# Kernel tuning notes

Measured on AMD Instinct MI355X. Metric: run time of the kernel, lower is better.

The kernel has to match this reference:

```python
import jax, jax.numpy as jnp
import numpy as np

B, S, D = 8, 2048, 512
FF = 2048
E = 8

def setup_inputs() -> dict:
    key = jax.random.key(0)
    ks = jax.random.split(key, 7)
    s = 1.0 / np.sqrt(D)
    sf = 1.0 / np.sqrt(FF)
    return {
        "x":  jax.random.normal(ks[0], (B, S, D), dtype=jnp.float32),
        "Wg": jax.random.uniform(ks[1], (D, E), jnp.float32, -s, s),
        "bg": jax.random.uniform(ks[2], (E,), jnp.float32, -s, s),
        "W1": jax.random.uniform(ks[3], (E, D, FF), jnp.float32, -s, s),
        "b1": jax.random.uniform(ks[4], (E, FF), jnp.float32, -s, s),
        "W2": jax.random.uniform(ks[5], (E, FF, D), jnp.float32, -sf, sf),
        "b2": jax.random.uniform(ks[6], (E, D), jnp.float32, -sf, sf),
    }

def reference(x, Wg, bg, W1, b1, W2, b2):
    b, s, d = x.shape
    xf = x.reshape(-1, d)                      # [T, D]
    logits = xf @ Wg + bg                      # [T, E]
    probs = jax.nn.softmax(logits, axis=-1)
    pmax = jnp.max(probs, axis=-1)             # [T]
    routes = jnp.argmax(probs, axis=-1)        # [T] int
    xs = xf * pmax[:, None]                    # scale tokens by router prob
    # per-expert FFN over all tokens, select the routed expert's output
    out_tok = jnp.zeros_like(xf)
    for e in range(E):
        h = jax.nn.relu(xs @ W1[e] + b1[e])    # [T, FF]
        y = h @ W2[e] + b2[e]                  # [T, D]
        out_tok = jnp.where((routes == e)[:, None], y, out_tok)
    # torch.cat of per-expert nonzero-index gathers == tokens stably sorted by expert id
    order = jnp.argsort(routes)                # jnp.argsort is stable
    return out_tok[order].reshape(b, s, d)
```

## Files before the change

### kernel.cpp

```cpp
#include <hip/hip_runtime.h>
#include <hip/hip_bf16.h>

constexpr int TTOK  = 16384;
constexpr int DDIM  = 512;
constexpr int FFDIM = 2048;
constexpr int NEXP  = 8;
constexpr int GB_TOK = 16;
constexpr int NGB    = TTOK / GB_TOK;
constexpr int MAXTILES = TTOK / 128 + NEXP;
constexpr int PREP_GATE = NGB;
constexpr int PREP_TR   = 16 * 1024;

typedef __attribute__((ext_vector_type(8))) short short8_t;
typedef __attribute__((ext_vector_type(4))) float f32x4_t;

__device__ __forceinline__ unsigned short f2bf(float f) {
    union { float f; unsigned u; } v; v.f = f;
    return (unsigned short)((v.u + 0x7fffu + ((v.u >> 16) & 1u)) >> 16);
}

__device__ __forceinline__ void gl_lds16(const void* g, void* l) {
    __builtin_amdgcn_global_load_lds(
        (const __attribute__((address_space(1))) void*)g,
        (__attribute__((address_space(3))) void*)l,
        16, 0, 0);
}

__global__ __launch_bounds__(256) void prep_kernel(const float* __restrict__ x,
                                                   const float* __restrict__ Wg,
                                                   const float* __restrict__ bg,
                                                   int* __restrict__ route,
                                                   float* __restrict__ pmax,
                                                   int* __restrict__ blockCounts,
                                                   const float* __restrict__ W1,
                                                   const float* __restrict__ W2,
                                                   unsigned short* __restrict__ W1T,
                                                   unsigned short* __restrict__ W2T) {
    int tid = threadIdx.x;
    if (blockIdx.x >= PREP_GATE) {
        __shared__ float tile[32][33];
        int id = blockIdx.x - PREP_GATE;
        int z = id >> 10;
        int t = id & 1023;
        bool isW2 = z >= NEXP;
        int e = isW2 ? z - NEXP : z;
        int R = isW2 ? FFDIM : DDIM;
        int C = isW2 ? DDIM : FFDIM;
        int tilesC = C / 32;
        int c0 = (t % tilesC) * 32;
        int r0 = (t / tilesC) * 32;
        const float* s = (isW2 ? W2 : W1) + (size_t)e * DDIM * FFDIM;
        unsigned short* d = (isW2 ? W2T : W1T) + (size_t)e * DDIM * FFDIM;
        int tx = tid & 31, ty = tid >> 5;
        #pragma unroll
        for (int i = 0; i < 4; i++)
            tile[ty + 8 * i][tx] = s[(size_t)(r0 + ty + 8 * i) * C + c0 + tx];
        __syncthreads();
        #pragma unroll
        for (int i = 0; i < 4; i++)
            d[(size_t)(c0 + ty + 8 * i) * R + r0 + tx] = f2bf(tile[tx][ty + 8 * i]);
        return;
    }
    __shared__ int cnt[NEXP];
    __shared__ float bgs[NEXP];
    int gb = blockIdx.x;
    if (tid < NEXP) { cnt[tid] = 0; bgs[tid] = bg[tid]; }
    __syncthreads();
    int wave = tid >> 6, lane = tid & 63;
    float w[8][8];
    #pragma unroll
    for (int jj = 0; jj < 8; jj++) {
        float4 a = *(const float4*)(Wg + (size_t)(lane * 8 + jj) * NEXP);
        float4 b = *(const float4*)(Wg + (size_t)(lane * 8 + jj) * NEXP + 4);
        w[jj][0] = a.x; w[jj][1] = a.y; w[jj][2] = a.z; w[jj][3] = a.w;
        w[jj][4] = b.x; w[jj][5] = b.y; w[jj][6] = b.z; w[jj][7] = b.w;
    }
    int tbase = gb * GB_TOK + wave * 4;
    for (int it = 0; it < 4; it++) {
        int t = tbase + it;
        float4 xa = *(const float4*)(x + (size_t)t * DDIM + lane * 8);
        float4 xb = *(const float4*)(x + (size_t)t * DDIM + lane * 8 + 4);
        float xs[8] = {xa.x, xa.y, xa.z, xa.w, xb.x, xb.y, xb.z, xb.w};
        double acc[NEXP];
        #pragma unroll
        for (int e = 0; e < NEXP; e++) acc[e] = 0.0;
        #pragma unroll
        for (int jj = 0; jj < 8; jj++) {
            double xv = (double)xs[jj];
            #pragma unroll
            for (int e = 0; e < NEXP; e++) acc[e] += xv * (double)w[jj][e];
        }
        #pragma unroll
        for (int off = 32; off > 0; off >>= 1) {
            #pragma unroll
            for (int e = 0; e < NEXP; e++) acc[e] += __shfl_down(acc[e], off);
        }
        if (lane == 0) {
            double l[NEXP];
            #pragma unroll
            for (int e = 0; e < NEXP; e++) l[e] = acc[e] + (double)bgs[e];
            int r = 0; double lm = l[0];
            #pragma unroll
            for (int e = 1; e < NEXP; e++) if (l[e] > lm) { lm = l[e]; r = e; }
            double s = 0.0;
            #pragma unroll
            for (int e = 0; e < NEXP; e++) s += exp(l[e] - lm);
            route[t] = r;
            pmax[t] = (float)(1.0 / s);
            atomicAdd(&cnt[r], 1);
        }
    }
    __syncthreads();
    if (tid < NEXP) blockCounts[gb * NEXP + tid] = cnt[tid];
}

__global__ __launch_bounds__(1024) void scan_kernel(const int* __restrict__ blockCounts,
                                                    int* __restrict__ blockOffsets,
                                                    int* __restrict__ segPrefix,
                                                    int* __restrict__ tilePrefix) {
    int b = threadIdx.x, lane = b & 63, wv = b >> 6;
    int c[NEXP], s[NEXP];
    #pragma unroll
    for (int e = 0; e < NEXP; e++) { c[e] = blockCounts[b * NEXP + e]; s[e] = c[e]; }
    #pragma unroll
    for (int off = 1; off < 64; off <<= 1) {
        #pragma unroll
        for (int e = 0; e < NEXP; e++) {
            int t = __shfl_up(s[e], off);
            if (lane >= off) s[e] += t;
        }
    }
    __shared__ int wtot[16][NEXP];
    __shared__ int wpre[16][NEXP];
    __shared__ int base[NEXP + 1];
    if (lane == 63) {
        #pragma unroll
        for (int e = 0; e < NEXP; e++) wtot[wv][e] = s[e];
    }
    __syncthreads();
    if (wv == 0) {
        int t[NEXP];
        #pragma unroll
        for (int e = 0; e < NEXP; e++) t[e] = (lane < 16) ? wtot[lane][e] : 0;
        #pragma unroll
        for (int off = 1; off < 16; off <<= 1) {
            #pragma unroll
            for (int e = 0; e < NEXP; e++) {
                int u = __shfl_up(t[e], off);
                if (lane >= off) t[e] += u;
            }
        }
        if (lane < 16) {
            #pragma unroll
            for (int e = 0; e < NEXP; e++) wpre[lane][e] = t[e] - wtot[lane][e];
        }
        if (lane == 15) {
            int ssum = 0;
            #pragma unroll
            for (int e = 0; e < NEXP; e++) { base[e] = ssum; segPrefix[e] = ssum; ssum += t[e]; }
            base[NEXP] = ssum; segPrefix[NEXP] = ssum;
            int tp = 0; tilePrefix[0] = 0;
            #pragma unroll
            for (int e = 0; e < NEXP; e++) { tp += (t[e] + 127) >> 7; tilePrefix[e + 1] = tp; }
        }
    }
    __syncthreads();
    #pragma unroll
    for (int e = 0; e < NEXP; e++)
        blockOffsets[b * NEXP + e] = base[e] + wpre[wv][e] + s[e] - c[e];
}

__global__ __launch_bounds__(256) void scatter_kernel(const float* __restrict__ x,
                                                      const int* __restrict__ route,
                                                      const float* __restrict__ pmax,
                                                      const int* __restrict__ blockOffsets,
                                                      unsigned short* __restrict__ Xs) {
    __shared__ int dstL[GB_TOK];
    __shared__ float pmL[GB_TOK];
    int tid = threadIdx.x;
    int bb = blockIdx.x;
    if (tid < GB_TOK) {
        int t = bb * GB_TOK + tid;
        int r = route[t];
        unsigned long long ltmask = (tid == 0) ? 0ull : ((~0ull) >> (64 - tid));
        int rank = 0;
        #pragma unroll
        for (int e = 0; e < NEXP; e++) {
            unsigned long long m = __ballot(r == e);
            if (r == e) rank = __popcll(m & ltmask);
        }
        dstL[tid] = blockOffsets[bb * NEXP + r] + rank;
        pmL[tid] = pmax[t];
    }
    __syncthreads();
    int wave = tid >> 6, lane = tid & 63;
    for (int rr = 0; rr < 4; rr++) {
        int rowl = wave * 4 + rr;
        int t = bb * GB_TOK + rowl;
        float pm = pmL[rowl];
        const float4* xr = (const float4*)(x + (size_t)t * DDIM) + lane * 2;
        float4 a = xr[0], b = xr[1];
        union { short8_t v; unsigned short s[8]; } o;
        o.s[0] = f2bf(a.x * pm); o.s[1] = f2bf(a.y * pm);
        o.s[2] = f2bf(a.z * pm); o.s[3] = f2bf(a.w * pm);
        o.s[4] = f2bf(b.x * pm); o.s[5] = f2bf(b.y * pm);
        o.s[6] = f2bf(b.z * pm); o.s[7] = f2bf(b.w * pm);
        *(short8_t*)(Xs + (size_t)dstL[rowl] * DDIM + lane * 8) = o.v;
    }
}

template <bool RELU, typename OutT, int K, int N>
__global__ __launch_bounds__(256) void gemm_seg(const unsigned short* __restrict__ A,
                                                const unsigned short* __restrict__ Bt,
                                                const float* __restrict__ bias,
                                                OutT* __restrict__ C,
                                                const int* __restrict__ segPrefix,
                                                const int* __restrict__ tilePrefix) {
    int bx = blockIdx.x;
    bx = (bx & 7) * (MAXTILES / 8) + (bx >> 3);
    int t = bx;
    if (t >= tilePrefix[NEXP]) return;
    int e = 0;
    #pragma unroll
    for (int i = 1; i <= NEXP; i++) e += (t >= tilePrefix[i]) ? 1 : 0;
    int seg1 = segPrefix[e + 1];
    int m0 = segPrefix[e] + (t - tilePrefix[e]) * 128;
    int n0 = blockIdx.y * 128;

    __shared__ unsigned short As[2 * 4096];
    __shared__ unsigned short Bs[2 * 4096];

    int tid = threadIdx.x, wave = tid >> 6, lane = tid & 63;
    const unsigned short* Bte = Bt + (size_t)e * N * K;

    int srow = lane >> 2;
    int sg   = (lane & 3) ^ ((lane >> 2) & 3) ^ ((lane >> 4) & 3);
    int scol = sg * 8;

    f32x4_t acc[4][4];
    #pragma unroll
    for (int i = 0; i < 4; i++)
        #pragma unroll
        for (int j = 0; j < 4; j++) acc[i][j] = (f32x4_t){0.f, 0.f, 0.f, 0.f};

    int wm = (wave & 1) * 64;
    int wn = (wave >> 1) * 64;
    int frow = lane & 15;
    int gr = lane >> 4;
    int fswz = (gr ^ (frow & 3) ^ ((frow >> 2) & 3)) * 8;

    int reg0 = wave * 2;
    int arow0 = m0 + reg0 * 16 + srow;
    arow0 = arow0 < TTOK ? arow0 : TTOK - 1;
    int arow1 = m0 + (reg0 + 1) * 16 + srow;
    arow1 = arow1 < TTOK ? arow1 : TTOK - 1;
    const unsigned short* aptr0 = A + (size_t)arow0 * K + scol;
    const unsigned short* aptr1 = A + (size_t)arow1 * K + scol;
    const unsigned short* bptr0 = Bte + (size_t)(n0 + reg0 * 16 + srow) * K + scol;
    const unsigned short* bptr1 = Bte + (size_t)(n0 + (reg0 + 1) * 16 + srow) * K + scol;

    #pragma unroll
    for (int kc = 0; kc < K; kc += 64) {
        #pragma unroll
        for (int p = 0; p < 2; p++) {
            gl_lds16(aptr0 + kc + p * 32, &As[p * 4096 + reg0 * 512]);
            gl_lds16(aptr1 + kc + p * 32, &As[p * 4096 + (reg0 + 1) * 512]);
            gl_lds16(bptr0 + kc + p * 32, &Bs[p * 4096 + reg0 * 512]);
            gl_lds16(bptr1 + kc + p * 32, &Bs[p * 4096 + (reg0 + 1) * 512]);
        }
        __syncthreads();
        #pragma unroll
        for (int p = 0; p < 2; p++) {
            short8_t af[4], bfr[4];
            #pragma unroll
            for (int i = 0; i < 4; i++)
                af[i] = *(const short8_t*)&As[p * 4096 + (wm + i * 16 + frow) * 32 + fswz];
            #pragma unroll
            for (int j = 0; j < 4; j++)
                bfr[j] = *(const short8_t*)&Bs[p * 4096 + (wn + j * 16 + frow) * 32 + fswz];
            #pragma unroll
            for (int i = 0; i < 4; i++)
                #pragma unroll
                for (int j = 0; j < 4; j++)
                    acc[i][j] = __builtin_amdgcn_mfma_f32_16x16x32_bf16(af[i], bfr[j], acc[i][j], 0, 0, 0);
        }
        __syncthreads();
    }

    int quad = lane >> 4;
    int colb = lane & 15;
    float bv[4];
    #pragma unroll
    for (int j = 0; j < 4; j++) bv[j] = bias[(size_t)e * N + n0 + wn + j * 16 + colb];

    if constexpr (sizeof(OutT) == 2) {
        unsigned short* cbuf = As;
        #pragma unroll
        for (int p = 0; p < 2; p++) {
            __syncthreads();
            if ((wave >> 1) == p) {
                #pragma unroll
                for (int i = 0; i < 4; i++)
                    #pragma unroll
                    for (int j = 0; j < 4; j++)
                        #pragma unroll
                        for (int r = 0; r < 4; r++) {
                            float v = acc[i][j][r] + bv[j];
                            if (RELU) v = fmaxf(v, 0.0f);
                            int wrow = wm + i * 16 + quad * 4 + r;
                            int cc = (j * 16 + colb) ^ (((wrow >> 3) & 1) * 16);
                            cbuf[wrow * 72 + cc] = f2bf(v);
                        }
            }
            __syncthreads();
            int row = tid >> 1, ch = (tid & 1) * 32;
            int grow = m0 + row;
            if (grow < seg1) {
                #pragma unroll
                for (int k = 0; k < 4; k++) {
                    int vv = (ch + k * 8) ^ (((row >> 3) & 1) * 16);
                    short8_t v = *(const short8_t*)&cbuf[row * 72 + vv];
                    *(short8_t*)&C[(size_t)grow * N + n0 + p * 64 + ch + k * 8] = v;
                }
            }
        }
    } else {
        #pragma unroll
        for (int i = 0; i < 4; i++) {
            #pragma unroll
            for (int j = 0; j < 4; j++) {
                int col = n0 + wn + j * 16 + colb;
                #pragma unroll
                for (int r = 0; r < 4; r++) {
                    int row = m0 + wm + i * 16 + quad * 4 + r;
                    if (row < seg1) {
                        float v = acc[i][j][r] + bv[j];
                        if (RELU) v = fmaxf(v, 0.0f);
                        C[(size_t)row * N + col] = v;
                    }
                }
            }
        }
    }
}

extern "C" void kernel_launch(void* const* d_in, const int* in_sizes, int n_in,
                              void* d_out, int out_size, void* d_ws, size_t ws_size,
                              hipStream_t stream) {
    const float* x  = (const float*)d_in[0];
    const float* Wg = (const float*)d_in[1];
    const float* bg = (const float*)d_in[2];
    const float* W1 = (const float*)d_in[3];
    const float* b1 = (const float*)d_in[4];
    const float* W2 = (const float*)d_in[5];
    const float* b2 = (const float*)d_in[6];
    float* out = (float*)d_out;

    char* ws = (char*)d_ws;
    size_t off = 0;
    auto alloc = [&](size_t bytes) -> char* {
        char* p = ws + off;
        off += (bytes + 255) & ~(size_t)255;
        return p;
    };
    unsigned short* W1T = (unsigned short*)alloc((size_t)NEXP * DDIM * FFDIM * 2);
    unsigned short* W2T = (unsigned short*)alloc((size_t)NEXP * DDIM * FFDIM * 2);
    unsigned short* Xs  = (unsigned short*)alloc((size_t)TTOK * DDIM * 2);
    unsigned short* H   = (unsigned short*)alloc((size_t)TTOK * FFDIM * 2);
    int*   route        = (int*)alloc((size_t)TTOK * 4);
    float* pmaxArr      = (float*)alloc((size_t)TTOK * 4);
    int*   blockCounts  = (int*)alloc((size_t)NGB * NEXP * 4);
    int*   blockOffsets = (int*)alloc((size_t)NGB * NEXP * 4);
    int*   segPrefix    = (int*)alloc((size_t)(NEXP + 1) * 4);
    int*   tilePrefix   = (int*)alloc((size_t)(NEXP + 1) * 4);

    prep_kernel<<<PREP_GATE + PREP_TR, 256, 0, stream>>>(
        x, Wg, bg, route, pmaxArr, blockCounts, W1, W2, W1T, W2T);
    scan_kernel<<<1, NGB, 0, stream>>>(blockCounts, blockOffsets, segPrefix, tilePrefix);
    scatter_kernel<<<NGB, 256, 0, stream>>>(x, route, pmaxArr, blockOffsets, Xs);
    gemm_seg<true, unsigned short, DDIM, FFDIM><<<dim3(MAXTILES, FFDIM / 128, 1), 256, 0, stream>>>(
        Xs, W1T, b1, H, segPrefix, tilePrefix);
    gemm_seg<false, float, FFDIM, DDIM><<<dim3(MAXTILES, DDIM / 128, 1), 256, 0, stream>>>(
        H, W2T, b2, out, segPrefix, tilePrefix);
}
```

Measured before the change: 311.2 us.

## Move W2 transpose into GEMM1 launch and widen transpose tiles

```diff
diff --git a/kernel.cpp b/kernel.cpp
--- a/kernel.cpp
+++ b/kernel.cpp
@@ -8,8 +8,8 @@
 constexpr int GB_TOK = 16;
 constexpr int NGB    = TTOK / GB_TOK;
 constexpr int MAXTILES = TTOK / 128 + NEXP;
-constexpr int PREP_GATE = NGB;
-constexpr int PREP_TR   = 16 * 1024;
+constexpr int TRW1_BLOCKS = 4096;
+constexpr int TRW2_XBLK   = 256;
 
 typedef __attribute__((ext_vector_type(8))) short short8_t;
 typedef __attribute__((ext_vector_type(4))) float f32x4_t;
@@ -24,6 +24,35 @@
         (const __attribute__((address_space(1))) void*)g,
         (__attribute__((address_space(3))) void*)l,
         16, 0, 0);
+}
+
+__device__ __forceinline__ void tr_tile(const float* __restrict__ src,
+                                        unsigned short* __restrict__ dst,
+                                        int R, int C, int tileId, float* lds) {
+    int tilesC = C / 32;
+    int c0 = (tileId % tilesC) * 32;
+    int r0 = (tileId / tilesC) * 64;
+    int t = threadIdx.x;
+    int lr = t >> 3;
+    int ls = t & 7;
+    #pragma unroll
+    for (int rb = 0; rb < 2; rb++) {
+        int row = rb * 32 + lr;
+        float4 v = *(const float4*)(src + (size_t)(r0 + row) * C + c0 + 4 * ls);
+        int p4 = (4 * ls) ^ (8 * ((row >> 3) & 3));
+        *(float4*)(lds + row * 36 + p4) = v;
+    }
+    __syncthreads();
+    int c = t >> 3;
+    int b = t & 7;
+    union { short8_t v; unsigned short s[8]; } o;
+    #pragma unroll
+    for (int j = 0; j < 8; j++) {
+        int r = 8 * b + j;
+        int p = c ^ (8 * ((r >> 3) & 3));
+        o.s[j] = f2bf(lds[r * 36 + p]);
+    }
+    *(short8_t*)(dst + (size_t)(c0 + c) * R + r0 + 8 * b) = o.v;
 }
 
 __global__ __launch_bounds__(256) void prep_kernel(const float* __restrict__ x,
@@ -33,32 +62,15 @@
                                                    float* __restrict__ pmax,
                                                    int* __restrict__ blockCounts,
                                                    const float* __restrict__ W1,
-                                                   const float* __restrict__ W2,
-                                                   unsigned short* __restrict__ W1T,
-                                                   unsigned short* __restrict__ W2T) {
+                                                   unsigned short* __restrict__ W1T) {
     int tid = threadIdx.x;
-    if (blockIdx.x >= PREP_GATE) {
-        __shared__ float tile[32][33];
-        int id = blockIdx.x - PREP_GATE;
-        int z = id >> 10;
-        int t = id & 1023;
-        bool isW2 = z >= NEXP;
-        int e = isW2 ? z - NEXP : z;
-        int R = isW2 ? FFDIM : DDIM;
-        int C = isW2 ? DDIM : FFDIM;
-        int tilesC = C / 32;
-        int c0 = (t % tilesC) * 32;
-        int r0 = (t / tilesC) * 32;
-        const float* s = (isW2 ? W2 : W1) + (size_t)e * DDIM * FFDIM;
-        unsigned short* d = (isW2 ? W2T : W1T) + (size_t)e * DDIM * FFDIM;
-        int tx = tid & 31, ty = tid >> 5;
-        #pragma unroll
-        for (int i = 0; i < 4; i++)
-            tile[ty + 8 * i][tx] = s[(size_t)(r0 + ty + 8 * i) * C + c0 + tx];
-        __syncthreads();
-        #pragma unroll
-        for (int i = 0; i < 4; i++)
-            d[(size_t)(c0 + ty + 8 * i) * R + r0 + tx] = f2bf(tile[tx][ty + 8 * i]);
+    if (blockIdx.x >= NGB) {
+        __shared__ __align__(16) float tlds[64 * 36];
+        int id = blockIdx.x - NGB;
+        int e = id >> 9;
+        int tile = id & 511;
+        tr_tile(W1 + (size_t)e * DDIM * FFDIM, W1T + (size_t)e * DDIM * FFDIM,
+                DDIM, FFDIM, tile, tlds);
         return;
     }
     __shared__ int cnt[NEXP];
@@ -209,6 +221,135 @@
     }
 }
 
+__global__ __launch_bounds__(256) void gemm1_fused(const unsigned short* __restrict__ A,
+                                                   const unsigned short* __restrict__ Bt,
+                                                   const float* __restrict__ bias,
+                                                   unsigned short* __restrict__ C,
+                                                   const int* __restrict__ segPrefix,
+                                                   const int* __restrict__ tilePrefix,
+                                                   const float* __restrict__ W2,
+                                                   unsigned short* __restrict__ W2T) {
+    constexpr int K = DDIM, N = FFDIM;
+    __shared__ __align__(16) unsigned short SMEM[16384];
+
+    if (blockIdx.x >= MAXTILES) {
+        int id = (blockIdx.x - MAXTILES) * 16 + blockIdx.y;
+        int e = id >> 9;
+        int tile = id & 511;
+        tr_tile(W2 + (size_t)e * DDIM * FFDIM, W2T + (size_t)e * DDIM * FFDIM,
+                FFDIM, DDIM, tile, (float*)SMEM);
+        return;
+    }
+
+    int bx = blockIdx.x;
+    bx = (bx & 7) * (MAXTILES / 8) + (bx >> 3);
+    int t = bx;
+    if (t >= tilePrefix[NEXP]) return;
+    int e = 0;
+    #pragma unroll
+    for (int i = 1; i <= NEXP; i++) e += (t >= tilePrefix[i]) ? 1 : 0;
+    int seg1 = segPrefix[e + 1];
+    int m0 = segPrefix[e] + (t - tilePrefix[e]) * 128;
+    int n0 = blockIdx.y * 128;
+
+    unsigned short* As = SMEM;
+    unsigned short* Bs = SMEM + 8192;
+
+    int tid = threadIdx.x, wave = tid >> 6, lane = tid & 63;
+    const unsigned short* Bte = Bt + (size_t)e * N * K;
+
+    int srow = lane >> 2;
+    int sg   = (lane & 3) ^ ((lane >> 2) & 3) ^ ((lane >> 4) & 3);
+    int scol = sg * 8;
+
+    f32x4_t acc[4][4];
+    #pragma unroll
+    for (int i = 0; i < 4; i++)
+        #pragma unroll
+        for (int j = 0; j < 4; j++) acc[i][j] = (f32x4_t){0.f, 0.f, 0.f, 0.f};
+
+    int wm = (wave & 1) * 64;
+    int wn = (wave >> 1) * 64;
+    int frow = lane & 15;
+    int gr = lane >> 4;
+    int fswz = (gr ^ (frow & 3) ^ ((frow >> 2) & 3)) * 8;
+
+    int reg0 = wave * 2;
+    int arow0 = m0 + reg0 * 16 + srow;
+    arow0 = arow0 < TTOK ? arow0 : TTOK - 1;
+    int arow1 = m0 + (reg0 + 1) * 16 + srow;
+    arow1 = arow1 < TTOK ? arow1 : TTOK - 1;
+    const unsigned short* aptr0 = A + (size_t)arow0 * K + scol;
+    const unsigned short* aptr1 = A + (size_t)arow1 * K + scol;
+    const unsigned short* bptr0 = Bte + (size_t)(n0 + reg0 * 16 + srow) * K + scol;
+    const unsigned short* bptr1 = Bte + (size_t)(n0 + (reg0 + 1) * 16 + srow) * K + scol;
+
+    #pragma unroll
+    for (int kc = 0; kc < K; kc += 64) {
+        #pragma unroll
+        for (int p = 0; p < 2; p++) {
+            gl_lds16(aptr0 + kc + p * 32, &As[p * 4096 + reg0 * 512]);
+            gl_lds16(aptr1 + kc + p * 32, &As[p * 4096 + (reg0 + 1) * 512]);
+            gl_lds16(bptr0 + kc + p * 32, &Bs[p * 4096 + reg0 * 512]);
+            gl_lds16(bptr1 + kc + p * 32, &Bs[p * 4096 + (reg0 + 1) * 512]);
+        }
+        __syncthreads();
+        #pragma unroll
+        for (int p = 0; p < 2; p++) {
+            short8_t af[4], bfr[4];
+            #pragma unroll
+            for (int i = 0; i < 4; i++)
+                af[i] = *(const short8_t*)&As[p * 4096 + (wm + i * 16 + frow) * 32 + fswz];
+            #pragma unroll
+            for (int j = 0; j < 4; j++)
+                bfr[j] = *(const short8_t*)&Bs[p * 4096 + (wn + j * 16 + frow) * 32 + fswz];
+            #pragma unroll
+            for (int i = 0; i < 4; i++)
+                #pragma unroll
+                for (int j = 0; j < 4; j++)
+                    acc[i][j] = __builtin_amdgcn_mfma_f32_16x16x32_bf16(af[i], bfr[j], acc[i][j], 0, 0, 0);
+        }
+        __syncthreads();
+    }
+
+    int quad = lane >> 4;
+    int colb = lane & 15;
+    float bv[4];
+    #pragma unroll
+    for (int j = 0; j < 4; j++) bv[j] = bias[(size_t)e * N + n0 + wn + j * 16 + colb];
+
+    unsigned short* cbuf = As;
+    #pragma unroll
+    for (int p = 0; p < 2; p++) {
+        __syncthreads();
+        if ((wave >> 1) == p) {
+            #pragma unroll
+            for (int i = 0; i < 4; i++)
+                #pragma unroll
+                for (int j = 0; j < 4; j++)
+                    #pragma unroll
+                    for (int r = 0; r < 4; r++) {
+                        float v = acc[i][j][r] + bv[j];
+                        v = fmaxf(v, 0.0f);
+                        int wrow = wm + i * 16 + quad * 4 + r;
+                        int cc = (j * 16 + colb) ^ (((wrow >> 3) & 1) * 16);
+                        cbuf[wrow * 72 + cc] = f2bf(v);
+                    }
+        }
+        __syncthreads();
+        int row = tid >> 1, ch = (tid & 1) * 32;
+        int grow = m0 + row;
+        if (grow < seg1) {
+            #pragma unroll
+            for (int k = 0; k < 4; k++) {
+                int vv = (ch + k * 8) ^ (((row >> 3) & 1) * 16);
+                short8_t v = *(const short8_t*)&cbuf[row * 72 + vv];
+                *(short8_t*)&C[(size_t)grow * N + n0 + p * 64 + ch + k * 8] = v;
+            }
+        }
+    }
+}
+
 template <bool RELU, typename OutT, int K, int N>
 __global__ __launch_bounds__(256) void gemm_seg(const unsigned short* __restrict__ A,
                                                 const unsigned short* __restrict__ Bt,
@@ -293,51 +434,18 @@
     #pragma unroll
     for (int j = 0; j < 4; j++) bv[j] = bias[(size_t)e * N + n0 + wn + j * 16 + colb];
 
-    if constexpr (sizeof(OutT) == 2) {
-        unsigned short* cbuf = As;
-        #pragma unroll
-        for (int p = 0; p < 2; p++) {
-            __syncthreads();
-            if ((wave >> 1) == p) {
-                #pragma unroll
-                for (int i = 0; i < 4; i++)
-                    #pragma unroll
-                    for (int j = 0; j < 4; j++)
-                        #pragma unroll
-                        for (int r = 0; r < 4; r++) {
-                            float v = acc[i][j][r] + bv[j];
-                            if (RELU) v = fmaxf(v, 0.0f);
-                            int wrow = wm + i * 16 + quad * 4 + r;
-                            int cc = (j * 16 + colb) ^ (((wrow >> 3) & 1) * 16);
-                            cbuf[wrow * 72 + cc] = f2bf(v);
-                        }
-            }
-            __syncthreads();
-            int row = tid >> 1, ch = (tid & 1) * 32;
-            int grow = m0 + row;
-            if (grow < seg1) {
-                #pragma unroll
-                for (int k = 0; k < 4; k++) {
-                    int vv = (ch + k * 8) ^ (((row >> 3) & 1) * 16);
-                    short8_t v = *(const short8_t*)&cbuf[row * 72 + vv];
-                    *(short8_t*)&C[(size_t)grow * N + n0 + p * 64 + ch + k * 8] = v;
-                }
-            }
-        }
-    } else {
-        #pragma unroll
-        for (int i = 0; i < 4; i++) {
-            #pragma unroll
-            for (int j = 0; j < 4; j++) {
-                int col = n0 + wn + j * 16 + colb;
-                #pragma unroll
-                for (int r = 0; r < 4; r++) {
-                    int row = m0 + wm + i * 16 + quad * 4 + r;
-                    if (row < seg1) {
-                        float v = acc[i][j][r] + bv[j];
-                        if (RELU) v = fmaxf(v, 0.0f);
-                        C[(size_t)row * N + col] = v;
-                    }
+    #pragma unroll
+    for (int i = 0; i < 4; i++) {
+        #pragma unroll
+        for (int j = 0; j < 4; j++) {
+            int col = n0 + wn + j * 16 + colb;
+            #pragma unroll
+            for (int r = 0; r < 4; r++) {
+                int row = m0 + wm + i * 16 + quad * 4 + r;
+                if (row < seg1) {
+                    float v = acc[i][j][r] + bv[j];
+                    if (RELU) v = fmaxf(v, 0.0f);
+                    C[(size_t)row * N + col] = v;
                 }
             }
         }
@@ -374,12 +482,12 @@
     int*   segPrefix    = (int*)alloc((size_t)(NEXP + 1) * 4);
     int*   tilePrefix   = (int*)alloc((size_t)(NEXP + 1) * 4);
 
-    prep_kernel<<<PREP_GATE + PREP_TR, 256, 0, stream>>>(
-        x, Wg, bg, route, pmaxArr, blockCounts, W1, W2, W1T, W2T);
+    prep_kernel<<<NGB + TRW1_BLOCKS, 256, 0, stream>>>(
+        x, Wg, bg, route, pmaxArr, blockCounts, W1, W1T);
     scan_kernel<<<1, NGB, 0, stream>>>(blockCounts, blockOffsets, segPrefix, tilePrefix);
     scatter_kernel<<<NGB, 256, 0, stream>>>(x, route, pmaxArr, blockOffsets, Xs);
-    gemm_seg<true, unsigned short, DDIM, FFDIM><<<dim3(MAXTILES, FFDIM / 128, 1), 256, 0, stream>>>(
-        Xs, W1T, b1, H, segPrefix, tilePrefix);
+    gemm1_fused<<<dim3(MAXTILES + TRW2_XBLK, FFDIM / 128, 1), 256, 0, stream>>>(
+        Xs, W1T, b1, H, segPrefix, tilePrefix, W2, W2T);
     gemm_seg<false, float, FFDIM, DDIM><<<dim3(MAXTILES, DDIM / 128, 1), 256, 0, stream>>>(
         H, W2T, b2, out, segPrefix, tilePrefix);
 }
```

New measurement: 294.5 us. 1.06x faster.
